# Kernel tuning notes

Hardware: AMD Instinct MI355X
Metric: run time of the kernel (lower is better)

## Reference

```python
import jax, jax.numpy as jnp
import numpy as np

C = 64          # residual channels
N_LAYERS = 30
MAX_STEPS = 200
SQRT2 = 2.0 ** 0.5


def _conv1d(x, W, b, dilation=1, pad=0):
    # x: [B, Cin, T], W: [Cout, Cin, K], b: [Cout]
    y = jax.lax.conv_general_dilated(
        x, W, window_strides=(1,), padding=[(pad, pad)],
        rhs_dilation=(dilation,), dimension_numbers=('NCH', 'OIH', 'NCH'))
    return y + b[None, :, None]


def _silu(x):
    return x * jax.nn.sigmoid(x)


def _emb_table():
    steps = jnp.arange(MAX_STEPS, dtype=jnp.float32)[:, None]      # [200,1]
    dims = jnp.arange(64, dtype=jnp.float32)[None, :]              # [1,64]
    t = steps * 10.0 ** (dims * 4.0 / 63.0)                        # [200,64]
    return jnp.concatenate([jnp.sin(t), jnp.cos(t)], axis=1)       # [200,128]


def setup_inputs() -> dict:
    key = jax.random.key(0)
    ks = jax.random.split(key, 20)
    B, T = 4, 16384
    f32 = jnp.float32
    inp = {
        'audio': jax.random.normal(ks[0], (B, 1, T), dtype=f32),
        'diffusion_step': jax.random.randint(ks[1], (B,), 0, MAX_STEPS),
        # input projection Conv1d(1, 64, 1)
        'in_W': jax.random.normal(ks[2], (C, 1, 1), f32) * 1.0,
        'in_b': jax.random.normal(ks[3], (C,), f32) * 0.01,
        # diffusion embedding MLP 128->512->512
        'p1_W': jax.random.normal(ks[4], (512, 128), f32) * (1.0 / np.sqrt(128)),
        'p1_b': jnp.zeros((512,), f32),
        'p2_W': jax.random.normal(ks[5], (512, 512), f32) * (1.0 / np.sqrt(512)),
        'p2_b': jnp.zeros((512,), f32),
        # per-layer params (stacked over 30 layers)
        'dw_W': jax.random.normal(ks[6], (N_LAYERS, 2 * C, C, 3), f32) * (1.0 / np.sqrt(3 * C)),
        'dw_b': jnp.zeros((N_LAYERS, 2 * C), f32),
        'dp_W': jax.random.normal(ks[7], (N_LAYERS, C, 512), f32) * (1.0 / np.sqrt(512)),
        'dp_b': jnp.zeros((N_LAYERS, C), f32),
        'op_W': jax.random.normal(ks[8], (N_LAYERS, 2 * C, C, 1), f32) * (1.0 / np.sqrt(C)),
        'op_b': jnp.zeros((N_LAYERS, 2 * C), f32),
        # skip projection Conv1d(64,64,1)
        'sk_W': jax.random.normal(ks[9], (C, C, 1), f32) * (1.0 / np.sqrt(C)),
        'sk_b': jnp.zeros((C,), f32),
        # output projection Conv1d(64,1,1), weight zero-init like original
        'out_W': jnp.zeros((1, C, 1), f32),
        'out_b': jax.random.normal(ks[10], (1,), f32) * 0.01,
    }
    return inp


def reference(audio, diffusion_step, in_W, in_b, p1_W, p1_b, p2_W, p2_b,
              dw_W, dw_b, dp_W, dp_b, op_W, op_b, sk_W, sk_b, out_W, out_b):
    x = jax.nn.relu(_conv1d(audio, in_W, in_b))                    # [B,64,T]
    # diffusion embedding
    t = _emb_table()[diffusion_step]                               # [B,128]
    t = _silu(t @ p1_W.T + p1_b)                                   # [B,512]
    t = _silu(t @ p2_W.T + p2_b)                                   # [B,512]
    skip = None
    for i in range(N_LAYERS):
        d = 2 ** (i % 10)
        cond = (t @ dp_W[i].T + dp_b[i])[:, :, None]               # [B,64,1]
        y = _conv1d(x + cond, dw_W[i], dw_b[i], dilation=d, pad=d) # [B,128,T]
        gate, filt = y[:, :C], y[:, C:]
        y = jax.nn.sigmoid(gate) * jnp.tanh(filt)                  # [B,64,T]
        y = _conv1d(y, op_W[i], op_b[i])                           # [B,128,T]
        residual, sk = y[:, :C], y[:, C:]
        x = (x + residual) / SQRT2
        skip = sk if skip is None else skip + sk
    x = skip / np.sqrt(float(N_LAYERS)).astype(np.float32)
    x = jax.nn.relu(_conv1d(x, sk_W, sk_b))
    return _conv1d(x, out_W, out_b)                                # [B,1,T]
```

## Files before the change

kernel.cpp:

```cpp
#include <hip/hip_runtime.h>
#include <math.h>

#define C 64
#define NL 30
#define T 16384
#define B 4

typedef __bf16 bf16_t;
typedef __bf16 bf16x8 __attribute__((ext_vector_type(8)));
typedef __bf16 bf16x4 __attribute__((ext_vector_type(4)));
typedef float f32x4 __attribute__((ext_vector_type(4)));

typedef const __attribute__((address_space(1))) unsigned int glb_u32;
typedef __attribute__((address_space(3))) unsigned int lds_u32;

constexpr float INV_SQRT2   = 0.70710678118654752440f;
constexpr float INV_SQRT_NL = 0.18257418583505537115f;

__device__ __forceinline__ float fsig(float x) {
    return __builtin_amdgcn_rcpf(1.f + __builtin_amdgcn_exp2f(-1.44269504089f * x));
}
__device__ __forceinline__ float ftanh(float x) {
    return fmaf(2.f, __builtin_amdgcn_rcpf(1.f + __builtin_amdgcn_exp2f(-2.88539008178f * x)), -1.f);
}
__device__ __forceinline__ int swz(int off) { return off ^ ((off >> 3) & 0x70); }

__global__ void pack_weights(const float* __restrict__ dw_W,
                             const float* __restrict__ op_W,
                             const float* __restrict__ sk_W,
                             bf16_t* __restrict__ convpk,
                             bf16_t* __restrict__ oppk,
                             bf16_t* __restrict__ skpk) {
    int idx = blockIdx.x * 256 + threadIdx.x;
    const int ndw = NL * 128 * 192;
    const int nop = NL * 128 * 64;
    if (idx < ndw) {
        int k = idx % 192; int r = idx / 192;
        int oc = r % 128;  int l = r / 128;
        int tap = k >> 6, ic = k & 63;
        convpk[idx] = (bf16_t)dw_W[((l * 128 + oc) * 64 + ic) * 3 + tap];
    } else if (idx < ndw + nop) {
        oppk[idx - ndw] = (bf16_t)op_W[idx - ndw];
    } else if (idx < ndw + nop + 4096) {
        int j = idx - ndw - nop;
        skpk[j] = (bf16_t)(sk_W[j] * INV_SQRT_NL);
    }
}

__global__ void cond_embp1(const int* __restrict__ step,
                           const float* __restrict__ p1_W, const float* __restrict__ p1_b,
                           float* __restrict__ h1out) {
    __shared__ float e[128];
    __shared__ float red[256];
    int b = blockIdx.x, blk = blockIdx.y, tid = threadIdx.x;
    int s = step[b];
    if (tid < 128) {
        int d = tid & 63;
        float tf = (float)s * powf(10.f, (float)d * 4.f / 63.f);
        double td = (double)tf;
        e[tid] = (tid < 64) ? (float)sin(td) : (float)cos(td);
    }
    __syncthreads();
    int ol = tid >> 2, q = tid & 3;
    int o = blk * 64 + ol;
    const float4* wr = (const float4*)(p1_W + o * 128 + q * 32);
    const float4* ev = (const float4*)(e + q * 32);
    float a = 0.f;
    #pragma unroll
    for (int j = 0; j < 8; ++j) {
        float4 wv = wr[j]; float4 xv = ev[j];
        a = fmaf(wv.x, xv.x, a); a = fmaf(wv.y, xv.y, a);
        a = fmaf(wv.z, xv.z, a); a = fmaf(wv.w, xv.w, a);
    }
    red[tid] = a;
    __syncthreads();
    if (q == 0) {
        float v = red[tid] + red[tid + 1] + red[tid + 2] + red[tid + 3] + p1_b[o];
        h1out[b * 512 + o] = v / (1.f + expf(-v));
    }
}

__global__ void cond_p2(const float* __restrict__ h1,
                        const float* __restrict__ p2_W, const float* __restrict__ p2_b,
                        float* __restrict__ h2out) {
    __shared__ float red[256];
    int b = blockIdx.x, blk = blockIdx.y, tid = threadIdx.x;
    int ol = tid >> 2, q = tid & 3;
    int o = blk * 64 + ol;
    const float4* wr = (const float4*)(p2_W + o * 512 + q * 128);
    const float4* hv = (const float4*)(h1 + b * 512 + q * 128);
    float a = 0.f;
    #pragma unroll 8
    for (int j = 0; j < 32; ++j) {
        float4 wv = wr[j]; float4 xv = hv[j];
        a = fmaf(wv.x, xv.x, a); a = fmaf(wv.y, xv.y, a);
        a = fmaf(wv.z, xv.z, a); a = fmaf(wv.w, xv.w, a);
    }
    red[tid] = a;
    __syncthreads();
    if (q == 0) {
        float v = red[tid] + red[tid + 1] + red[tid + 2] + red[tid + 3] + p2_b[o];
        h2out[b * 512 + o] = v / (1.f + expf(-v));
    }
}

__global__ void cond_stage2b(const float* __restrict__ h2,
                             const float* __restrict__ dp_W, const float* __restrict__ dp_b,
                             const bf16_t* __restrict__ convpk,
                             const float* __restrict__ dw_b,
                             float* __restrict__ bias2) {
    __shared__ float red[256];
    __shared__ float cond_s[64];
    int l = blockIdx.x, b = blockIdx.y;
    int tid = threadIdx.x;
    {
        int o = tid >> 2, q = tid & 3;
        const float4* wr = (const float4*)(dp_W + ((size_t)l * C + o) * 512 + q * 128);
        const float4* h = (const float4*)(h2 + b * 512 + q * 128);
        float a = 0.f;
        #pragma unroll 8
        for (int j = 0; j < 32; ++j) {
            float4 wv = wr[j]; float4 hv = h[j];
            a = fmaf(wv.x, hv.x, a); a = fmaf(wv.y, hv.y, a);
            a = fmaf(wv.z, hv.z, a); a = fmaf(wv.w, hv.w, a);
        }
        red[tid] = a;
        __syncthreads();
        if (q == 0)
            cond_s[o] = red[tid] + red[tid + 1] + red[tid + 2] + red[tid + 3] + dp_b[l * C + o];
    }
    __syncthreads();
    int oc = tid & 127, kh = tid >> 7;
    const bf16_t* wr = convpk + ((size_t)l * 128 + oc) * 192 + kh * 96;
    float a = kh ? 0.f : dw_b[l * 128 + oc];
    #pragma unroll
    for (int j = 0; j < 96; ++j)
        a = fmaf((float)wr[j], cond_s[(kh * 96 + j) & 63], a);
    __syncthreads();
    red[tid] = a;
    __syncthreads();
    if (tid < 128)
        bias2[(l * B + b) * 128 + tid] = red[tid] + red[tid + 128];
}

__global__ __launch_bounds__(256) void in_conv(
    const float* __restrict__ audio,
    const float* __restrict__ in_W, const float* __restrict__ in_b,
    bf16_t* __restrict__ x)
{
    int bid = blockIdx.x;
    int tile = ((bid & 7) << 4) + (bid >> 3);
    int b = blockIdx.y;
    int t0 = tile * 128;
    int tid = threadIdx.x;
    #pragma unroll
    for (int r = 0; r < 4; ++r) {
        int q = r * 256 + tid;
        int row = q >> 3, c16 = q & 7;
        float av = audio[(size_t)b * T + t0 + row];
        bf16x8 o;
        #pragma unroll
        for (int j = 0; j < 8; ++j) {
            int c = c16 * 8 + j;
            o[j] = (bf16_t)fmaxf(fmaf(in_W[c], av, in_b[c]), 0.f);
        }
        *(bf16x8*)(x + ((size_t)b * T + t0 + row) * 64 + c16 * 8) = o;
    }
}

__global__ __launch_bounds__(256) void layer_kernel(
    const bf16_t* __restrict__ x_in, bf16_t* __restrict__ x_out, bf16_t* __restrict__ skip,
    const bf16_t* __restrict__ convpk, const bf16_t* __restrict__ oppk,
    const float* __restrict__ bias2, const float* __restrict__ op_b,
    const bf16_t* __restrict__ zpage,
    int layer, int dil, int first)
{
    __shared__ uint4 smem_u[2048];
    char* sm = (char*)smem_u;

    int tid = threadIdx.x;
    int w = __builtin_amdgcn_readfirstlane(tid >> 6);
    int l = tid & 63;
    int lr = l & 15;
    int g = l >> 4;
    int b = blockIdx.y;
    int bid = blockIdx.x;
    int tile = ((bid & 7) << 4) + (bid >> 3);
    int tbase = tile * 128;
    const bf16_t* xb = x_in + (size_t)b * T * 64;

    bf16x8 cA[2][6];
    const bf16_t* cw = convpk + (size_t)layer * 128 * 192;
    #pragma unroll
    for (int mf = 0; mf < 2; ++mf)
        #pragma unroll
        for (int kf = 0; kf < 6; ++kf)
            cA[mf][kf] = *(const bf16x8*)(cw + (mf * 64 + w * 16 + lr) * 192 + kf * 32 + g * 8);
    bf16x8 oA[2][2];
    const bf16_t* ow = oppk + (size_t)layer * 128 * 64;
    #pragma unroll
    for (int mf = 0; mf < 2; ++mf)
        #pragma unroll
        for (int kf = 0; kf < 2; ++kf)
            oA[mf][kf] = *(const bf16x8*)(ow + (mf * 64 + w * 16 + lr) * 64 + kf * 32 + g * 8);
    f32x4 bC[2], bO[2];
    const float* b2 = bias2 + (layer * B + b) * 128;
    const float* ob = op_b + layer * 2 * C;
    #pragma unroll
    for (int mf = 0; mf < 2; ++mf)
        #pragma unroll
        for (int r = 0; r < 4; ++r) {
            bC[mf][r] = b2[mf * 64 + w * 16 + g * 4 + r];
            bO[mf][r] = ob[mf * 64 + w * 16 + g * 4 + r];
        }

    size_t bb = (size_t)b * T * 64;

    for (int st = 0; st < 2; ++st) {
        int t0 = tbase + st * 64;

        #pragma unroll
        for (int it = 0; it < 6; ++it) {
            int qq = it * 256 + tid;
            int slice = qq >> 9, row = (qq >> 3) & 63, c16 = qq & 7;
            int ts = t0 + row + (slice - 1) * dil;
            int c16s = c16 ^ (row & 7);
            const bf16_t* src = ((unsigned)ts < (unsigned)T)
                ? (xb + (size_t)ts * 64 + c16s * 8)
                : (zpage + c16s * 8);
            __builtin_amdgcn_global_load_lds((glb_u32*)src,
                (lds_u32*)(sm + it * 4096 + w * 1024), 16, 0, 0);
        }
        __syncthreads();

        f32x4 acc[2][4];
        #pragma unroll
        for (int mf = 0; mf < 2; ++mf)
            #pragma unroll
            for (int nf = 0; nf < 4; ++nf) acc[mf][nf] = bC[mf];
        #pragma unroll
        for (int kf = 0; kf < 6; ++kf) {
            int tap = kf >> 1;
            int kc = (kf & 1) * 32;
            bf16x8 Bf[4];
            #pragma unroll
            for (int nf = 0; nf < 4; ++nf) {
                int off = tap * 8192 + (nf * 16 + lr) * 128 + (kc + g * 8) * 2;
                Bf[nf] = *(const bf16x8*)(sm + swz(off));
            }
            #pragma unroll
            for (int mf = 0; mf < 2; ++mf)
                #pragma unroll
                for (int nf = 0; nf < 4; ++nf)
                    acc[mf][nf] = __builtin_amdgcn_mfma_f32_16x16x32_bf16(
                        cA[mf][kf], Bf[nf], acc[mf][nf], 0, 0, 0);
        }

        #pragma unroll
        for (int nf = 0; nf < 4; ++nf) {
            union { bf16_t hh[4]; uint2 u; } zp;
            #pragma unroll
            for (int r = 0; r < 4; ++r)
                zp.hh[r] = (bf16_t)(fsig(acc[0][nf][r]) * ftanh(acc[1][nf][r]));
            int off = 24576 + (nf * 16 + lr) * 128 + (w * 16 + g * 4) * 2;
            *(uint2*)(sm + swz(off)) = zp.u;
        }
        __syncthreads();

        f32x4 acc2[2][4];
        #pragma unroll
        for (int mf = 0; mf < 2; ++mf)
            #pragma unroll
            for (int nf = 0; nf < 4; ++nf) acc2[mf][nf] = bO[mf];
        #pragma unroll
        for (int kf = 0; kf < 2; ++kf) {
            bf16x8 Zf[4];
            #pragma unroll
            for (int nf = 0; nf < 4; ++nf) {
                int off = 24576 + (nf * 16 + lr) * 128 + (kf * 32 + g * 8) * 2;
                Zf[nf] = *(const bf16x8*)(sm + swz(off));
            }
            #pragma unroll
            for (int mf = 0; mf < 2; ++mf)
                #pragma unroll
                for (int nf = 0; nf < 4; ++nf)
                    acc2[mf][nf] = __builtin_amdgcn_mfma_f32_16x16x32_bf16(
                        oA[mf][kf], Zf[nf], acc2[mf][nf], 0, 0, 0);
        }

        #pragma unroll
        for (int nf = 0; nf < 4; ++nf) {
            int t = t0 + nf * 16 + lr;
            int c0 = w * 16 + g * 4;
            int xoff = 8192 + (nf * 16 + lr) * 128 + c0 * 2;
            bf16x4 xv = *(const bf16x4*)(sm + swz(xoff));
            bf16x4 ro, so;
            bf16_t* sp = skip + bb + (size_t)t * 64 + c0;
            if (first) {
                #pragma unroll
                for (int r = 0; r < 4; ++r) {
                    ro[r] = (bf16_t)(((float)xv[r] + acc2[0][nf][r]) * INV_SQRT2);
                    so[r] = (bf16_t)acc2[1][nf][r];
                }
            } else {
                bf16x4 sv = *(const bf16x4*)sp;
                #pragma unroll
                for (int r = 0; r < 4; ++r) {
                    ro[r] = (bf16_t)(((float)xv[r] + acc2[0][nf][r]) * INV_SQRT2);
                    so[r] = (bf16_t)((float)sv[r] + acc2[1][nf][r]);
                }
            }
            *(bf16x4*)(x_out + bb + (size_t)t * 64 + c0) = ro;
            *(bf16x4*)sp = so;
        }
        if (st == 0) __syncthreads();
    }
}

__global__ __launch_bounds__(256) void final_kernel(
    const bf16_t* __restrict__ skip, const bf16_t* __restrict__ skpk,
    const float* __restrict__ sk_b,
    const float* __restrict__ out_W, const float* __restrict__ out_b,
    float* __restrict__ out)
{
    __shared__ uint4 tile_u[512];
    __shared__ float part[16][66];
    unsigned char* sm = (unsigned char*)tile_u;
    int tid = threadIdx.x;
    int w = __builtin_amdgcn_readfirstlane(tid >> 6);
    int l = tid & 63, lr = l & 15, g = l >> 4;
    int bid = blockIdx.x;
    int tile = ((bid & 7) << 5) + (bid >> 3);
    int b = blockIdx.y, t0 = tile * 64;
    const bf16_t* sb = skip + (size_t)b * T * 64;

    #pragma unroll
    for (int it = 0; it < 2; ++it) {
        int q = it * 256 + tid;
        int row = q >> 3, c16 = q & 7;
        uint4 val = *(const uint4*)(sb + (size_t)(t0 + row) * 64 + c16 * 8);
        *(uint4*)(sm + swz(row * 128 + c16 * 16)) = val;
    }

    bf16x8 aS[2];
    #pragma unroll
    for (int kf = 0; kf < 2; ++kf)
        aS[kf] = *(const bf16x8*)(skpk + (w * 16 + lr) * 64 + kf * 32 + g * 8);
    f32x4 acc[4];
    #pragma unroll
    for (int nf = 0; nf < 4; ++nf)
        #pragma unroll
        for (int r = 0; r < 4; ++r) acc[nf][r] = sk_b[w * 16 + g * 4 + r];
    __syncthreads();

    #pragma unroll
    for (int kf = 0; kf < 2; ++kf) {
        bf16x8 Bf[4];
        #pragma unroll
        for (int nf = 0; nf < 4; ++nf) {
            int off = (nf * 16 + lr) * 128 + (kf * 32 + g * 8) * 2;
            Bf[nf] = *(const bf16x8*)(sm + swz(off));
        }
        #pragma unroll
        for (int nf = 0; nf < 4; ++nf)
            acc[nf] = __builtin_amdgcn_mfma_f32_16x16x32_bf16(aS[kf], Bf[nf], acc[nf], 0, 0, 0);
    }

    #pragma unroll
    for (int nf = 0; nf < 4; ++nf) {
        float o = 0.f;
        #pragma unroll
        for (int r = 0; r < 4; ++r)
            o = fmaf(out_W[w * 16 + g * 4 + r], fmaxf(acc[nf][r], 0.f), o);
        part[w * 4 + g][nf * 16 + lr] = o;
    }
    __syncthreads();
    if (tid < 64) {
        float o = out_b[0];
        #pragma unroll
        for (int j = 0; j < 16; ++j) o += part[j][tid];
        out[(size_t)b * T + t0 + tid] = o;
    }
}

extern "C" void kernel_launch(void* const* d_in, const int* in_sizes, int n_in,
                              void* d_out, int out_size, void* d_ws, size_t ws_size,
                              hipStream_t stream) {
    const float* audio = (const float*)d_in[0];
    const int*   dstep = (const int*)d_in[1];
    const float* in_W  = (const float*)d_in[2];
    const float* in_b  = (const float*)d_in[3];
    const float* p1_W  = (const float*)d_in[4];
    const float* p1_b  = (const float*)d_in[5];
    const float* p2_W  = (const float*)d_in[6];
    const float* p2_b  = (const float*)d_in[7];
    const float* dw_W  = (const float*)d_in[8];
    const float* dw_b  = (const float*)d_in[9];
    const float* dp_W  = (const float*)d_in[10];
    const float* dp_b  = (const float*)d_in[11];
    const float* op_W  = (const float*)d_in[12];
    const float* op_b  = (const float*)d_in[13];
    const float* sk_W  = (const float*)d_in[14];
    const float* sk_b  = (const float*)d_in[15];
    const float* out_W = (const float*)d_in[16];
    const float* out_b = (const float*)d_in[17];

    float* ws = (float*)d_ws;
    const size_t NXE = (size_t)B * T * 64;
    float* h1    = ws;
    float* h2    = h1 + B * 512;
    float* bias2 = h2 + B * 512;
    float* zpg   = bias2 + NL * B * 128;
    bf16_t* xA   = (bf16_t*)(zpg + 128);
    bf16_t* xB   = xA + NXE;
    bf16_t* skip = xB + NXE;
    bf16_t* convpk = skip + NXE;
    bf16_t* oppk   = convpk + (size_t)NL * 128 * 192;
    bf16_t* skpk   = oppk + (size_t)NL * 128 * 64;

    hipMemsetAsync(zpg, 0, 512, stream);
    hipLaunchKernelGGL(pack_weights, dim3(3856), dim3(256), 0, stream,
                       dw_W, op_W, sk_W, convpk, oppk, skpk);
    hipLaunchKernelGGL(cond_embp1, dim3(B, 8), dim3(256), 0, stream,
                       dstep, p1_W, p1_b, h1);
    hipLaunchKernelGGL(cond_p2, dim3(B, 8), dim3(256), 0, stream,
                       h1, p2_W, p2_b, h2);
    hipLaunchKernelGGL(cond_stage2b, dim3(NL, B), dim3(256), 0, stream,
                       h2, dp_W, dp_b, convpk, dw_b, bias2);
    hipLaunchKernelGGL(in_conv, dim3(128, B), dim3(256), 0, stream,
                       audio, in_W, in_b, xA);

    bf16_t* bufs[2] = { xA, xB };
    int cur = 0;
    const bf16_t* zpgc = (const bf16_t*)zpg;
    for (int i = 0; i < NL; ++i) {
        int dil = 1 << (i % 10);
        hipLaunchKernelGGL(layer_kernel, dim3(128, B), dim3(256), 0, stream,
                           bufs[cur], bufs[cur ^ 1], skip, convpk, oppk,
                           bias2, op_b, zpgc, i, dil, (i == 0) ? 1 : 0);
        cur ^= 1;
    }
    hipLaunchKernelGGL(final_kernel, dim3(256, B), dim3(256), 0, stream,
                       skip, skpk, sk_b, out_W, out_b, (float*)d_out);
}
```

Before: 475.9 us.

## Fuse input conv into first layer and use one 64-step tile per block

Removes the separate in_conv kernel; layer 0 now computes the ReLU input projection from audio directly into shared memory for all three taps. Each layer block now handles a single 64-timestep tile, doubling the grid to 256xB blocks instead of looping twice per block. Weight and bias register loads are moved after the async LDS loads are issued, so they overlap. This saves one launch and a full x write/read, and raises parallelism at the cost of loading weights twice as often per timestep.

```diff
diff --git a/kernel.cpp b/kernel.cpp
--- a/kernel.cpp
+++ b/kernel.cpp
@@ -143,36 +143,14 @@
         bias2[(l * B + b) * 128 + tid] = red[tid] + red[tid + 128];
 }
 
-__global__ __launch_bounds__(256) void in_conv(
-    const float* __restrict__ audio,
-    const float* __restrict__ in_W, const float* __restrict__ in_b,
-    bf16_t* __restrict__ x)
-{
-    int bid = blockIdx.x;
-    int tile = ((bid & 7) << 4) + (bid >> 3);
-    int b = blockIdx.y;
-    int t0 = tile * 128;
-    int tid = threadIdx.x;
-    #pragma unroll
-    for (int r = 0; r < 4; ++r) {
-        int q = r * 256 + tid;
-        int row = q >> 3, c16 = q & 7;
-        float av = audio[(size_t)b * T + t0 + row];
-        bf16x8 o;
-        #pragma unroll
-        for (int j = 0; j < 8; ++j) {
-            int c = c16 * 8 + j;
-            o[j] = (bf16_t)fmaxf(fmaf(in_W[c], av, in_b[c]), 0.f);
-        }
-        *(bf16x8*)(x + ((size_t)b * T + t0 + row) * 64 + c16 * 8) = o;
-    }
-}
-
+template<int FROMAUD>
 __global__ __launch_bounds__(256) void layer_kernel(
     const bf16_t* __restrict__ x_in, bf16_t* __restrict__ x_out, bf16_t* __restrict__ skip,
     const bf16_t* __restrict__ convpk, const bf16_t* __restrict__ oppk,
     const float* __restrict__ bias2, const float* __restrict__ op_b,
     const bf16_t* __restrict__ zpage,
+    const float* __restrict__ audio,
+    const float* __restrict__ in_W, const float* __restrict__ in_b,
     int layer, int dil, int first)
 {
     __shared__ uint4 smem_u[2048];
@@ -185,40 +163,32 @@
     int g = l >> 4;
     int b = blockIdx.y;
     int bid = blockIdx.x;
-    int tile = ((bid & 7) << 4) + (bid >> 3);
-    int tbase = tile * 128;
+    int tile = ((bid & 7) << 5) + (bid >> 3);
+    int t0 = tile * 64;
     const bf16_t* xb = x_in + (size_t)b * T * 64;
-
-    bf16x8 cA[2][6];
-    const bf16_t* cw = convpk + (size_t)layer * 128 * 192;
-    #pragma unroll
-    for (int mf = 0; mf < 2; ++mf)
-        #pragma unroll
-        for (int kf = 0; kf < 6; ++kf)
-            cA[mf][kf] = *(const bf16x8*)(cw + (mf * 64 + w * 16 + lr) * 192 + kf * 32 + g * 8);
-    bf16x8 oA[2][2];
-    const bf16_t* ow = oppk + (size_t)layer * 128 * 64;
-    #pragma unroll
-    for (int mf = 0; mf < 2; ++mf)
-        #pragma unroll
-        for (int kf = 0; kf < 2; ++kf)
-            oA[mf][kf] = *(const bf16x8*)(ow + (mf * 64 + w * 16 + lr) * 64 + kf * 32 + g * 8);
-    f32x4 bC[2], bO[2];
-    const float* b2 = bias2 + (layer * B + b) * 128;
-    const float* ob = op_b + layer * 2 * C;
-    #pragma unroll
-    for (int mf = 0; mf < 2; ++mf)
-        #pragma unroll
-        for (int r = 0; r < 4; ++r) {
-            bC[mf][r] = b2[mf * 64 + w * 16 + g * 4 + r];
-            bO[mf][r] = ob[mf * 64 + w * 16 + g * 4 + r];
-        }
-
     size_t bb = (size_t)b * T * 64;
 
-    for (int st = 0; st < 2; ++st) {
-        int t0 = tbase + st * 64;
-
+    if constexpr (FROMAUD) {
+        #pragma unroll
+        for (int it = 0; it < 6; ++it) {
+            int q = it * 256 + tid;
+            int slice = q >> 9, row = (q >> 3) & 63, c16 = q & 7;
+            int ts = t0 + row + (slice - 1);
+            bf16x8 o;
+            if ((unsigned)ts < (unsigned)T) {
+                float av = audio[(size_t)b * T + ts];
+                #pragma unroll
+                for (int j = 0; j < 8; ++j) {
+                    int c = c16 * 8 + j;
+                    o[j] = (bf16_t)fmaxf(fmaf(in_W[c], av, in_b[c]), 0.f);
+                }
+            } else {
+                #pragma unroll
+                for (int j = 0; j < 8; ++j) o[j] = (bf16_t)0.f;
+            }
+            *(bf16x8*)(sm + swz(slice * 8192 + row * 128 + c16 * 16)) = o;
+        }
+    } else {
         #pragma unroll
         for (int it = 0; it < 6; ++it) {
             int qq = it * 256 + tid;
@@ -231,89 +201,113 @@
             __builtin_amdgcn_global_load_lds((glb_u32*)src,
                 (lds_u32*)(sm + it * 4096 + w * 1024), 16, 0, 0);
         }
-        __syncthreads();
-
-        f32x4 acc[2][4];
+    }
+
+    bf16x8 cA[2][6];
+    const bf16_t* cw = convpk + (size_t)layer * 128 * 192;
+    #pragma unroll
+    for (int mf = 0; mf < 2; ++mf)
+        #pragma unroll
+        for (int kf = 0; kf < 6; ++kf)
+            cA[mf][kf] = *(const bf16x8*)(cw + (mf * 64 + w * 16 + lr) * 192 + kf * 32 + g * 8);
+    bf16x8 oA[2][2];
+    const bf16_t* ow = oppk + (size_t)layer * 128 * 64;
+    #pragma unroll
+    for (int mf = 0; mf < 2; ++mf)
+        #pragma unroll
+        for (int kf = 0; kf < 2; ++kf)
+            oA[mf][kf] = *(const bf16x8*)(ow + (mf * 64 + w * 16 + lr) * 64 + kf * 32 + g * 8);
+    f32x4 bC[2], bO[2];
+    const float* b2 = bias2 + (layer * B + b) * 128;
+    const float* ob = op_b + layer * 2 * C;
+    #pragma unroll
+    for (int mf = 0; mf < 2; ++mf)
+        #pragma unroll
+        for (int r = 0; r < 4; ++r) {
+            bC[mf][r] = b2[mf * 64 + w * 16 + g * 4 + r];
+            bO[mf][r] = ob[mf * 64 + w * 16 + g * 4 + r];
+        }
+    __syncthreads();
+
+    f32x4 acc[2][4];
+    #pragma unroll
+    for (int mf = 0; mf < 2; ++mf)
+        #pragma unroll
+        for (int nf = 0; nf < 4; ++nf) acc[mf][nf] = bC[mf];
+    #pragma unroll
+    for (int kf = 0; kf < 6; ++kf) {
+        int tap = kf >> 1;
+        int kc = (kf & 1) * 32;
+        bf16x8 Bf[4];
+        #pragma unroll
+        for (int nf = 0; nf < 4; ++nf) {
+            int off = tap * 8192 + (nf * 16 + lr) * 128 + (kc + g * 8) * 2;
+            Bf[nf] = *(const bf16x8*)(sm + swz(off));
+        }
         #pragma unroll
         for (int mf = 0; mf < 2; ++mf)
             #pragma unroll
-            for (int nf = 0; nf < 4; ++nf) acc[mf][nf] = bC[mf];
-        #pragma unroll
-        for (int kf = 0; kf < 6; ++kf) {
-            int tap = kf >> 1;
-            int kc = (kf & 1) * 32;
-            bf16x8 Bf[4];
-            #pragma unroll
-            for (int nf = 0; nf < 4; ++nf) {
-                int off = tap * 8192 + (nf * 16 + lr) * 128 + (kc + g * 8) * 2;
-                Bf[nf] = *(const bf16x8*)(sm + swz(off));
-            }
-            #pragma unroll
-            for (int mf = 0; mf < 2; ++mf)
-                #pragma unroll
-                for (int nf = 0; nf < 4; ++nf)
-                    acc[mf][nf] = __builtin_amdgcn_mfma_f32_16x16x32_bf16(
-                        cA[mf][kf], Bf[nf], acc[mf][nf], 0, 0, 0);
-        }
-
+            for (int nf = 0; nf < 4; ++nf)
+                acc[mf][nf] = __builtin_amdgcn_mfma_f32_16x16x32_bf16(
+                    cA[mf][kf], Bf[nf], acc[mf][nf], 0, 0, 0);
+    }
+
+    #pragma unroll
+    for (int nf = 0; nf < 4; ++nf) {
+        union { bf16_t hh[4]; uint2 u; } zp;
+        #pragma unroll
+        for (int r = 0; r < 4; ++r)
+            zp.hh[r] = (bf16_t)(fsig(acc[0][nf][r]) * ftanh(acc[1][nf][r]));
+        int off = 24576 + (nf * 16 + lr) * 128 + (w * 16 + g * 4) * 2;
+        *(uint2*)(sm + swz(off)) = zp.u;
+    }
+    __syncthreads();
+
+    f32x4 acc2[2][4];
+    #pragma unroll
+    for (int mf = 0; mf < 2; ++mf)
+        #pragma unroll
+        for (int nf = 0; nf < 4; ++nf) acc2[mf][nf] = bO[mf];
+    #pragma unroll
+    for (int kf = 0; kf < 2; ++kf) {
+        bf16x8 Zf[4];
         #pragma unroll
         for (int nf = 0; nf < 4; ++nf) {
-            union { bf16_t hh[4]; uint2 u; } zp;
-            #pragma unroll
-            for (int r = 0; r < 4; ++r)
-                zp.hh[r] = (bf16_t)(fsig(acc[0][nf][r]) * ftanh(acc[1][nf][r]));
-            int off = 24576 + (nf * 16 + lr) * 128 + (w * 16 + g * 4) * 2;
-            *(uint2*)(sm + swz(off)) = zp.u;
-        }
-        __syncthreads();
-
-        f32x4 acc2[2][4];
+            int off = 24576 + (nf * 16 + lr) * 128 + (kf * 32 + g * 8) * 2;
+            Zf[nf] = *(const bf16x8*)(sm + swz(off));
+        }
         #pragma unroll
         for (int mf = 0; mf < 2; ++mf)
             #pragma unroll
-            for (int nf = 0; nf < 4; ++nf) acc2[mf][nf] = bO[mf];
-        #pragma unroll
-        for (int kf = 0; kf < 2; ++kf) {
-            bf16x8 Zf[4];
+            for (int nf = 0; nf < 4; ++nf)
+                acc2[mf][nf] = __builtin_amdgcn_mfma_f32_16x16x32_bf16(
+                    oA[mf][kf], Zf[nf], acc2[mf][nf], 0, 0, 0);
+    }
+
+    #pragma unroll
+    for (int nf = 0; nf < 4; ++nf) {
+        int t = t0 + nf * 16 + lr;
+        int c0 = w * 16 + g * 4;
+        int xoff = 8192 + (nf * 16 + lr) * 128 + c0 * 2;
+        bf16x4 xv = *(const bf16x4*)(sm + swz(xoff));
+        bf16x4 ro, so;
+        bf16_t* sp = skip + bb + (size_t)t * 64 + c0;
+        if (first) {
             #pragma unroll
-            for (int nf = 0; nf < 4; ++nf) {
-                int off = 24576 + (nf * 16 + lr) * 128 + (kf * 32 + g * 8) * 2;
-                Zf[nf] = *(const bf16x8*)(sm + swz(off));
+            for (int r = 0; r < 4; ++r) {
+                ro[r] = (bf16_t)(((float)xv[r] + acc2[0][nf][r]) * INV_SQRT2);
+                so[r] = (bf16_t)acc2[1][nf][r];
             }
+        } else {
+            bf16x4 sv = *(const bf16x4*)sp;
             #pragma unroll
-            for (int mf = 0; mf < 2; ++mf)
-                #pragma unroll
-                for (int nf = 0; nf < 4; ++nf)
-                    acc2[mf][nf] = __builtin_amdgcn_mfma_f32_16x16x32_bf16(
-                        oA[mf][kf], Zf[nf], acc2[mf][nf], 0, 0, 0);
-        }
-
-        #pragma unroll
-        for (int nf = 0; nf < 4; ++nf) {
-            int t = t0 + nf * 16 + lr;
-            int c0 = w * 16 + g * 4;
-            int xoff = 8192 + (nf * 16 + lr) * 128 + c0 * 2;
-            bf16x4 xv = *(const bf16x4*)(sm + swz(xoff));
-            bf16x4 ro, so;
-            bf16_t* sp = skip + bb + (size_t)t * 64 + c0;
-            if (first) {
-                #pragma unroll
-                for (int r = 0; r < 4; ++r) {
-                    ro[r] = (bf16_t)(((float)xv[r] + acc2[0][nf][r]) * INV_SQRT2);
-                    so[r] = (bf16_t)acc2[1][nf][r];
-                }
-            } else {
-                bf16x4 sv = *(const bf16x4*)sp;
-                #pragma unroll
-                for (int r = 0; r < 4; ++r) {
-                    ro[r] = (bf16_t)(((float)xv[r] + acc2[0][nf][r]) * INV_SQRT2);
-                    so[r] = (bf16_t)((float)sv[r] + acc2[1][nf][r]);
-                }
+            for (int r = 0; r < 4; ++r) {
+                ro[r] = (bf16_t)(((float)xv[r] + acc2[0][nf][r]) * INV_SQRT2);
+                so[r] = (bf16_t)((float)sv[r] + acc2[1][nf][r]);
             }
-            *(bf16x4*)(x_out + bb + (size_t)t * 64 + c0) = ro;
-            *(bf16x4*)sp = so;
-        }
-        if (st == 0) __syncthreads();
+        }
+        *(bf16x4*)(x_out + bb + (size_t)t * 64 + c0) = ro;
+        *(bf16x4*)sp = so;
     }
 }
 
@@ -427,17 +421,21 @@
                        h1, p2_W, p2_b, h2);
     hipLaunchKernelGGL(cond_stage2b, dim3(NL, B), dim3(256), 0, stream,
                        h2, dp_W, dp_b, convpk, dw_b, bias2);
-    hipLaunchKernelGGL(in_conv, dim3(128, B), dim3(256), 0, stream,
-                       audio, in_W, in_b, xA);
 
     bf16_t* bufs[2] = { xA, xB };
     int cur = 0;
     const bf16_t* zpgc = (const bf16_t*)zpg;
     for (int i = 0; i < NL; ++i) {
         int dil = 1 << (i % 10);
-        hipLaunchKernelGGL(layer_kernel, dim3(128, B), dim3(256), 0, stream,
-                           bufs[cur], bufs[cur ^ 1], skip, convpk, oppk,
-                           bias2, op_b, zpgc, i, dil, (i == 0) ? 1 : 0);
+        if (i == 0) {
+            hipLaunchKernelGGL((layer_kernel<1>), dim3(256, B), dim3(256), 0, stream,
+                               bufs[cur], bufs[cur ^ 1], skip, convpk, oppk,
+                               bias2, op_b, zpgc, audio, in_W, in_b, 0, 1, 1);
+        } else {
+            hipLaunchKernelGGL((layer_kernel<0>), dim3(256, B), dim3(256), 0, stream,
+                               bufs[cur], bufs[cur ^ 1], skip, convpk, oppk,
+                               bias2, op_b, zpgc, audio, in_W, in_b, i, dil, 0);
+        }
         cur ^= 1;
     }
     hipLaunchKernelGGL(final_kernel, dim3(256, B), dim3(256), 0, stream,
```

Measured after the change: 549.2 us. +15.4%, slower.
